# Kernel optimization log

Measured on AMD Instinct MI355X. Metric: run time of the kernel, lower is better.

## Reference

```python
import jax, jax.numpy as jnp
import numpy as np

EMB = 1024
HID = 1536
NE = 8


def setup_inputs() -> dict:
    key = jax.random.key(0)
    ks = jax.random.split(key, 8)
    B, N, E, H, ne = 4, 2048, EMB, HID, NE
    s = 1.0 / np.sqrt(E)
    sh = 1.0 / np.sqrt(H)
    return {
        "x": jax.random.normal(ks[0], (B, N, E), dtype=jnp.float32),
        "Wr": jax.random.uniform(ks[1], (E, ne), minval=-s, maxval=s, dtype=jnp.float32),
        "br": jax.random.uniform(ks[2], (ne,), minval=-s, maxval=s, dtype=jnp.float32),
        "W1": jax.random.uniform(ks[3], (ne, E, H), minval=-s, maxval=s, dtype=jnp.float32),
        "b1": jax.random.uniform(ks[4], (ne, H), minval=-s, maxval=s, dtype=jnp.float32),
        "W2": jax.random.uniform(ks[5], (ne, H, E), minval=-sh, maxval=sh, dtype=jnp.float32),
        "b2": jax.random.uniform(ks[6], (ne, E), minval=-sh, maxval=sh, dtype=jnp.float32),
        "k": 2,
    }


def reference(x, Wr, br, W1, b1, W2, b2, k):
    B, N, E = x.shape
    T = B * N
    ne = Wr.shape[1]
    flat = x.reshape(T, E)
    logits = flat @ Wr + br                      # [T, ne]
    _, topk_idx = jax.lax.top_k(logits, k)       # [T, k]
    # counts[t, e] = number of top-k slots of token t assigned to expert e
    counts = jax.nn.one_hot(topk_idx, ne, dtype=flat.dtype).sum(axis=1)  # [T, ne]
    out = jnp.zeros_like(flat)
    for e in range(ne):  # small fixed loop over experts (structurally distinct weights)
        h = jax.nn.gelu(flat @ W1[e] + b1[e], approximate=False)  # torch nn.GELU = exact erf
        y = h @ W2[e] + b2[e]
        out = out + counts[:, e:e + 1] * y
    out = out / k
    return out.reshape(B, N, E)
```

## Files before the change

### kernel.cpp

```cpp
#include <hip/hip_runtime.h>
#include <hip/hip_bf16.h>
#include <math.h>

#define T_TOK 8192
#define EMB   1024
#define HID   1536
#define NE    8
#define NBINB 64
#define BINTOK (T_TOK / NBINB)

typedef float  floatx4 __attribute__((ext_vector_type(4)));
typedef __bf16 bf16x8  __attribute__((ext_vector_type(8)));

#define WS_COUNTS   0
#define WS_OFFSETS  1024
#define WS_FLAGS    2048
#define WS_BHIST    4096
#define WS_TOKMAP   8192
#define WS_TOKLIST  270336
#define WS_YBUF     532480
#define WS_W1T      34086912
#define WS_W2T      59252736
#define WS_H        84418560
#define WS_NEEDED   135143424

__device__ __forceinline__ float eload(const void* p, size_t idx, bool f32) {
  return f32 ? ((const float*)p)[idx] : (float)(((const __bf16*)p)[idx]);
}

__device__ __forceinline__ void glds16(const void* g, void* l) {
  __builtin_amdgcn_global_load_lds(
      (const __attribute__((address_space(1))) unsigned int*)g,
      (__attribute__((address_space(3))) unsigned int*)l, 16, 0, 0);
}

__global__ __launch_bounds__(256)
void sniff_kernel(const void* p0, const void* p1, const void* p2, const void* p3,
                  const void* p4, const void* p5, const void* p6, int* flags) {
  const void* ps[7] = {p0, p1, p2, p3, p4, p5, p6};
  const int nelem[7] = {T_TOK * EMB, EMB * NE, NE, NE * EMB * HID, NE * HID, NE * HID * EMB, NE * EMB};
  int t = blockIdx.x;
  const unsigned* w = (const unsigned*)ps[t];
  int nw = nelem[t] / 2;
  if (nw > 2048) nw = 2048;
  __shared__ int s_pl, s_nz;
  if (threadIdx.x == 0) { s_pl = 0; s_nz = 0; }
  __syncthreads();
  int pl = 0, nz = 0;
  for (int i = threadIdx.x; i < nw; i += 256) {
    unsigned v = w[i];
    if (v == 0) continue;
    nz++;
    unsigned e = (v >> 23) & 0xFF;
    if (e >= 100 && e <= 150) pl++;
  }
  atomicAdd(&s_pl, pl);
  atomicAdd(&s_nz, nz);
  __syncthreads();
  if (threadIdx.x == 0) flags[t] = (2 * s_pl > s_nz) ? 1 : 0;
}

__global__ __launch_bounds__(256)
void logits_kernel(const void* __restrict__ x, const void* __restrict__ Wr,
                   const void* __restrict__ br, const int* __restrict__ kptr,
                   const int* __restrict__ flags, int* __restrict__ topk,
                   __bf16* __restrict__ xbf) {
  const bool xf32  = flags[0] != 0;
  const bool wrf32 = flags[1] != 0;
  const bool brf32 = flags[2] != 0;
  const int wave = threadIdx.x >> 6;
  const int lane = threadIdx.x & 63;
  const int t = blockIdx.x * 4 + wave;

  float xv[16];
  {
    size_t base = (size_t)t * EMB + lane * 16;
    if (xf32) {
      const float* g = (const float*)x + base;
#pragma unroll
      for (int j = 0; j < 16; ++j) xv[j] = g[j];
    } else {
      bf16x8 u = *(const bf16x8*)((const __bf16*)x + base);
      bf16x8 v = *(const bf16x8*)((const __bf16*)x + base + 8);
#pragma unroll
      for (int j = 0; j < 8; ++j) { xv[j] = (float)u[j]; xv[8 + j] = (float)v[j]; }
    }
  }
  {
    bf16x8 o0, o1;
#pragma unroll
    for (int j = 0; j < 8; ++j) { o0[j] = (__bf16)xv[j]; o1[j] = (__bf16)xv[8 + j]; }
    __bf16* xo = xbf + (size_t)t * EMB + lane * 16;
    *(bf16x8*)xo = o0;
    *(bf16x8*)(xo + 8) = o1;
  }
  float acc[NE];
#pragma unroll
  for (int e = 0; e < NE; ++e) acc[e] = 0.f;
  if (wrf32) {
#pragma unroll
    for (int j = 0; j < 16; ++j) {
      const float* wr = (const float*)Wr + (size_t)(lane * 16 + j) * NE;
#pragma unroll
      for (int e = 0; e < NE; ++e) acc[e] += xv[j] * wr[e];
    }
  } else {
#pragma unroll
    for (int j = 0; j < 16; ++j) {
      bf16x8 wr = *(const bf16x8*)((const __bf16*)Wr + (size_t)(lane * 16 + j) * NE);
#pragma unroll
      for (int e = 0; e < NE; ++e) acc[e] += xv[j] * (float)wr[e];
    }
  }
#pragma unroll
  for (int e = 0; e < NE; ++e) {
#pragma unroll
    for (int off = 32; off > 0; off >>= 1)
      acc[e] += __shfl_xor(acc[e], off, 64);
  }
  if (lane == 0) {
    int k = kptr[0];
    if (k < 1) k = 1; if (k > NE) k = NE;
    float lg[NE];
#pragma unroll
    for (int e = 0; e < NE; ++e) lg[e] = acc[e] + eload(br, e, brf32);
    for (int s = 0; s < k; ++s) {
      int bi = 0; float bv = lg[0];
#pragma unroll
      for (int e = 1; e < NE; ++e) { if (lg[e] > bv) { bv = lg[e]; bi = e; } }
      lg[bi] = -3.0e38f;
      topk[t * 8 + s] = bi;
    }
  }
}

__global__ __launch_bounds__(128)
void bin1_kernel(const int* __restrict__ topk, const int* __restrict__ kptr,
                 int* __restrict__ bhist) {
  __shared__ int lhist[NE];
  if (threadIdx.x < NE) lhist[threadIdx.x] = 0;
  __syncthreads();
  int k = kptr[0];
  if (k < 1) k = 1; if (k > NE) k = NE;
  const int t = blockIdx.x * BINTOK + threadIdx.x;
  for (int s = 0; s < k; ++s) atomicAdd(&lhist[topk[t * 8 + s] & 7], 1);
  __syncthreads();
  if (threadIdx.x < NE) bhist[blockIdx.x * NE + threadIdx.x] = lhist[threadIdx.x];
}

__global__ __launch_bounds__(256)
void scan_kernel(int* __restrict__ bhist, int* __restrict__ counts, int* __restrict__ offsets) {
  __shared__ int sh[NBINB * NE];
  __shared__ int scnt[NE];
  __shared__ int soff[NE + 1];
  const int tid = threadIdx.x;
  for (int i = tid; i < NBINB * NE; i += 256) sh[i] = bhist[i];
  __syncthreads();
  if (tid < NE) {
    int s = 0;
    for (int b = 0; b < NBINB; ++b) s += sh[b * NE + tid];
    scnt[tid] = s;
  }
  __syncthreads();
  if (tid == 0) {
    int s = 0;
    for (int e = 0; e < NE; ++e) { soff[e] = s; s += scnt[e]; }
    soff[NE] = s;
  }
  __syncthreads();
  if (tid < NE) {
    int run = soff[tid];
    for (int b = 0; b < NBINB; ++b) {
      int v = sh[b * NE + tid];
      sh[b * NE + tid] = run;
      run += v;
    }
  }
  __syncthreads();
  for (int i = tid; i < NBINB * NE; i += 256) bhist[i] = sh[i];
  if (tid < NE) counts[tid] = scnt[tid];
  if (tid < NE + 1) offsets[tid] = soff[tid];
}

__global__ __launch_bounds__(128)
void bin2_kernel(const int* __restrict__ bhist, const int* __restrict__ offsets,
                 const int* __restrict__ kptr,
                 int* __restrict__ tok_list, int* __restrict__ tokmap) {
  __shared__ int lbase[NE];
  __shared__ int lcnt[NE];
  if (threadIdx.x < NE) {
    lbase[threadIdx.x] = bhist[blockIdx.x * NE + threadIdx.x];
    lcnt[threadIdx.x] = 0;
  }
  __syncthreads();
  int k = kptr[0];
  if (k < 1) k = 1; if (k > NE) k = NE;
  const int t = blockIdx.x * BINTOK + threadIdx.x;
  for (int s = 0; s < k; ++s) {
    int e = tokmap[t * 8 + s] & 7;
    int pos = atomicAdd(&lcnt[e], 1);
    int grow = lbase[e] + pos;
    tok_list[e * T_TOK + (grow - offsets[e])] = t;
    tokmap[t * 8 + s] = (e << 16) | grow;
  }
}

__global__ __launch_bounds__(256)
void transpose2_kernel(const void* __restrict__ W1, const void* __restrict__ W2,
                       __bf16* __restrict__ w1t, __bf16* __restrict__ w2t,
                       const int* __restrict__ flags) {
  const int z = blockIdx.z;
  const void* in; __bf16* out; int K, N; bool f32;
  if (z < 8) { in = W1; out = w1t; K = EMB; N = HID; f32 = flags[3] != 0; }
  else       { in = W2; out = w2t; K = HID; N = EMB; f32 = flags[5] != 0; }
  if ((int)blockIdx.x * 64 >= N || (int)blockIdx.y * 64 >= K) return;
  __shared__ __bf16 tile[64][65];
  size_t eoff = (size_t)(z & 7) * (size_t)K * (size_t)N;
  int n0 = blockIdx.x * 64;
  int k0 = blockIdx.y * 64;
  int tx = threadIdx.x & 63;
  int ty = threadIdx.x >> 6;
#pragma unroll
  for (int i = 0; i < 16; ++i) {
    int r = i * 4 + ty;
    tile[r][tx] = (__bf16)eload(in, eoff + (size_t)(k0 + r) * N + (n0 + tx), f32);
  }
  __syncthreads();
#pragma unroll
  for (int i = 0; i < 16; ++i) {
    int r = i * 4 + ty;
    out[eoff + (size_t)(n0 + r) * K + (k0 + tx)] = tile[tx][r];
  }
}


__global__ __launch_bounds__(256, 4)
void gemm1_kernel(const __bf16* __restrict__ xbf, const __bf16* __restrict__ w1t,
                  const void* __restrict__ b1, const int* __restrict__ counts,
                  const int* __restrict__ offsets, const int* __restrict__ tok_list,
                  const int* __restrict__ flags, __bf16* __restrict__ hbuf) {
  const int flat = blockIdx.x;
  const int e   = flat & 7;
  const int idx = flat >> 3;
  const int g   = idx / 12;
  const int nT  = idx % 12;
  const int cnt = counts[e];
  const bool b1f32 = flags[4] != 0;

  __shared__ __align__(16) __bf16 As[128 * 32];
  __shared__ __align__(16) __bf16 Bs[128 * 32];

  const int wave = threadIdx.x >> 6;
  const int lane = threadIdx.x & 63;
  const int sr = lane >> 2;
  const int r0 = wave * 16 + sr;
  const int r1 = 64 + wave * 16 + sr;
  const int cg = (lane & 3) ^ ((r0 >> 1) & 3);

  const __bf16* pB0base = w1t + ((size_t)e * HID + nT * 128 + r0) * EMB + cg * 8;
  const __bf16* pB1base = w1t + ((size_t)e * HID + nT * 128 + r1) * EMB + cg * 8;

  __bf16* dA0 = As + wave * 512;
  __bf16* dA1 = As + 2048 + wave * 512;
  __bf16* dB0 = Bs + wave * 512;
  __bf16* dB1 = Bs + 2048 + wave * 512;

  const int wm = (wave & 1) * 64;
  const int wn = (wave >> 1) * 64;
  const int fr = lane & 15;
  const int fc = lane >> 4;
  int aOff[4], bOff[4];
#pragma unroll
  for (int i = 0; i < 4; ++i) { int R = wm + i * 16 + fr; aOff[i] = R * 64 + ((fc ^ ((R >> 1) & 3)) << 4); }
#pragma unroll
  for (int j = 0; j < 4; ++j) { int R = wn + j * 16 + fr; bOff[j] = R * 64 + ((fc ^ ((R >> 1) & 3)) << 4); }

  const int colBase = nT * 128 + wn + fr;
  float bv[4];
#pragma unroll
  for (int j = 0; j < 4; ++j) bv[j] = eload(b1, (size_t)e * HID + colBase + j * 16, b1f32);

  for (int mT = g; mT * 128 < cnt; mT += 16) {
    const int tokA0 = tok_list[e * T_TOK + mT * 128 + r0];
    const int tokA1 = tok_list[e * T_TOK + mT * 128 + r1];
    const __bf16* pA0 = xbf + (size_t)tokA0 * EMB + cg * 8;
    const __bf16* pA1 = xbf + (size_t)tokA1 * EMB + cg * 8;
    const __bf16* pB0 = pB0base;
    const __bf16* pB1 = pB1base;

    floatx4 acc[4][4];
#pragma unroll
    for (int i = 0; i < 4; ++i)
#pragma unroll
      for (int j = 0; j < 4; ++j) acc[i][j] = (floatx4){0.f, 0.f, 0.f, 0.f};

    for (int kb = 0; kb < EMB / 32; ++kb) {
      __syncthreads();
      glds16(pA0, dA0); glds16(pA1, dA1);
      glds16(pB0, dB0); glds16(pB1, dB1);
      pA0 += 32; pA1 += 32; pB0 += 32; pB1 += 32;
      __syncthreads();
      bf16x8 af[4], bfr[4];
#pragma unroll
      for (int i = 0; i < 4; ++i) af[i]  = *(const bf16x8*)((const char*)As + aOff[i]);
#pragma unroll
      for (int j = 0; j < 4; ++j) bfr[j] = *(const bf16x8*)((const char*)Bs + bOff[j]);
#pragma unroll
      for (int i = 0; i < 4; ++i)
#pragma unroll
        for (int j = 0; j < 4; ++j)
          acc[i][j] = __builtin_amdgcn_mfma_f32_16x16x32_bf16(af[i], bfr[j], acc[i][j], 0, 0, 0);
    }

    const int hBase = offsets[e] + mT * 128;
#pragma unroll
    for (int i = 0; i < 4; ++i) {
      const int rowLoc = wm + i * 16 + fc * 4;
#pragma unroll
      for (int r = 0; r < 4; ++r) {
        const int row = rowLoc + r;
        if (mT * 128 + row < cnt) {
          __bf16* hp = hbuf + (size_t)(hBase + row) * HID + colBase;
#pragma unroll
          for (int j = 0; j < 4; ++j) {
            float v = acc[i][j][r] + bv[j];
            float gl = 0.5f * v * (1.0f + erff(v * 0.70710678118654752f));
            hp[j * 16] = (__bf16)gl;
          }
        }
      }
    }
  }
}

__global__ __launch_bounds__(256, 4)
void gemm2_kernel(const __bf16* __restrict__ hbuf, const __bf16* __restrict__ w2t,
                  const void* __restrict__ b2, const int* __restrict__ counts,
                  const int* __restrict__ offsets, const int* __restrict__ flags,
                  __bf16* __restrict__ ybuf) {
  const int flat = blockIdx.x;
  const int e   = flat & 7;
  const int idx = flat >> 3;
  const int g   = idx >> 3;
  const int nT  = idx & 7;
  const int cnt = counts[e];
  const bool b2f32 = flags[6] != 0;

  __shared__ __align__(16) __bf16 As[128 * 32];
  __shared__ __align__(16) __bf16 Bs[128 * 32];

  const int wave = threadIdx.x >> 6;
  const int lane = threadIdx.x & 63;
  const int sr = lane >> 2;
  const int r0 = wave * 16 + sr;
  const int r1 = 64 + wave * 16 + sr;
  const int cg = (lane & 3) ^ ((r0 >> 1) & 3);

  const __bf16* pB0base = w2t + ((size_t)e * EMB + nT * 128 + r0) * HID + cg * 8;
  const __bf16* pB1base = w2t + ((size_t)e * EMB + nT * 128 + r1) * HID + cg * 8;

  __bf16* dA0 = As + wave * 512;
  __bf16* dA1 = As + 2048 + wave * 512;
  __bf16* dB0 = Bs + wave * 512;
  __bf16* dB1 = Bs + 2048 + wave * 512;

  const int wm = (wave & 1) * 64;
  const int wn = (wave >> 1) * 64;
  const int fr = lane & 15;
  const int fc = lane >> 4;
  int aOff[4], bOff[4];
#pragma unroll
  for (int i = 0; i < 4; ++i) { int R = wm + i * 16 + fr; aOff[i] = R * 64 + ((fc ^ ((R >> 1) & 3)) << 4); }
#pragma unroll
  for (int j = 0; j < 4; ++j) { int R = wn + j * 16 + fr; bOff[j] = R * 64 + ((fc ^ ((R >> 1) & 3)) << 4); }

  const int colBase = nT * 128 + wn + fr;
  float bv[4];
#pragma unroll
  for (int j = 0; j < 4; ++j) bv[j] = eload(b2, (size_t)e * EMB + colBase + j * 16, b2f32);

  for (int mT = g; mT * 128 < cnt; mT += 16) {
    const int rowBase = offsets[e] + mT * 128;
    const __bf16* pA0 = hbuf + (size_t)(rowBase + r0) * HID + cg * 8;
    const __bf16* pA1 = hbuf + (size_t)(rowBase + r1) * HID + cg * 8;
    const __bf16* pB0 = pB0base;
    const __bf16* pB1 = pB1base;

    floatx4 acc[4][4];
#pragma unroll
    for (int i = 0; i < 4; ++i)
#pragma unroll
      for (int j = 0; j < 4; ++j) acc[i][j] = (floatx4){0.f, 0.f, 0.f, 0.f};

    for (int kb = 0; kb < HID / 32; ++kb) {
      __syncthreads();
      glds16(pA0, dA0); glds16(pA1, dA1);
      glds16(pB0, dB0); glds16(pB1, dB1);
      pA0 += 32; pA1 += 32; pB0 += 32; pB1 += 32;
      __syncthreads();
      bf16x8 af[4], bfr[4];
#pragma unroll
      for (int i = 0; i < 4; ++i) af[i]  = *(const bf16x8*)((const char*)As + aOff[i]);
#pragma unroll
      for (int j = 0; j < 4; ++j) bfr[j] = *(const bf16x8*)((const char*)Bs + bOff[j]);
#pragma unroll
      for (int i = 0; i < 4; ++i)
#pragma unroll
        for (int j = 0; j < 4; ++j)
          acc[i][j] = __builtin_amdgcn_mfma_f32_16x16x32_bf16(af[i], bfr[j], acc[i][j], 0, 0, 0);
    }

#pragma unroll
    for (int i = 0; i < 4; ++i) {
      const int rowLoc = wm + i * 16 + fc * 4;
#pragma unroll
      for (int r = 0; r < 4; ++r) {
        const int row = rowLoc + r;
        if (mT * 128 + row < cnt) {
          __bf16* yp = ybuf + (size_t)(rowBase + row) * EMB + colBase;
#pragma unroll
          for (int j = 0; j < 4; ++j)
            yp[j * 16] = (__bf16)(acc[i][j][r] + bv[j]);
        }
      }
    }
  }
}

__global__ __launch_bounds__(256)
void combine_kernel(const __bf16* __restrict__ ybuf, const int* __restrict__ tokmap,
                    const int* __restrict__ kptr, const int* __restrict__ flags,
                    void* __restrict__ out) {
  const bool f32 = flags[0] != 0;
  const int wave = threadIdx.x >> 6;
  const int lane = threadIdx.x & 63;
  const int t = blockIdx.x * 4 + wave;
  int k = kptr[0];
  if (k < 1) k = 1; if (k > NE) k = NE;
  const float invk = 1.0f / (float)k;
  int rows[NE];
  for (int s = 0; s < k; ++s) rows[s] = tokmap[t * 8 + s] & 0xFFFF;
#pragma unroll
  for (int c = 0; c < 2; ++c) {
    const int i = c * 512 + lane * 8;
    float a[8];
#pragma unroll
    for (int j = 0; j < 8; ++j) a[j] = 0.f;
    for (int s = 0; s < k; ++s) {
      bf16x8 y = *(const bf16x8*)(ybuf + (size_t)rows[s] * EMB + i);
#pragma unroll
      for (int j = 0; j < 8; ++j) a[j] += (float)y[j];
    }
    if (f32) {
      float* op = (float*)out + (size_t)t * EMB + i;
      float4 u = {a[0] * invk, a[1] * invk, a[2] * invk, a[3] * invk};
      float4 v = {a[4] * invk, a[5] * invk, a[6] * invk, a[7] * invk};
      *(float4*)op = u;
      *(float4*)(op + 4) = v;
    } else {
      bf16x8 o;
#pragma unroll
      for (int j = 0; j < 8; ++j) o[j] = (__bf16)(a[j] * invk);
      *(bf16x8*)((__bf16*)out + (size_t)t * EMB + i) = o;
    }
  }
}

extern "C" void kernel_launch(void* const* d_in, const int* in_sizes, int n_in,
                              void* d_out, int out_size, void* d_ws, size_t ws_size,
                              hipStream_t stream) {
  (void)in_sizes; (void)n_in; (void)out_size;
  if (ws_size < (size_t)WS_NEEDED) return;

  const void* x  = d_in[0];
  const void* Wr = d_in[1];
  const void* br = d_in[2];
  const void* W1 = d_in[3];
  const void* b1 = d_in[4];
  const void* W2 = d_in[5];
  const void* b2 = d_in[6];
  const int* kptr = (const int*)d_in[7];

  char* ws = (char*)d_ws;
  int*    counts   = (int*)(ws + WS_COUNTS);
  int*    offsets  = (int*)(ws + WS_OFFSETS);
  int*    flags    = (int*)(ws + WS_FLAGS);
  int*    bhist    = (int*)(ws + WS_BHIST);
  int*    tokmap   = (int*)(ws + WS_TOKMAP);
  int*    tok_list = (int*)(ws + WS_TOKLIST);
  __bf16* ybuf     = (__bf16*)(ws + WS_YBUF);
  __bf16* xbf      = (__bf16*)(ws + WS_YBUF);
  __bf16* w1t      = (__bf16*)(ws + WS_W1T);
  __bf16* w2t      = (__bf16*)(ws + WS_W2T);
  __bf16* hbuf     = (__bf16*)(ws + WS_H);

  hipMemsetAsync(ws + WS_TOKLIST, 0, NE * T_TOK * 4, stream);

  sniff_kernel<<<dim3(7), 256, 0, stream>>>(x, Wr, br, W1, b1, W2, b2, flags);

  transpose2_kernel<<<dim3(HID / 64, HID / 64, 16), 256, 0, stream>>>(W1, W2, w1t, w2t, flags);

  logits_kernel<<<dim3(T_TOK / 4), 256, 0, stream>>>(x, Wr, br, kptr, flags, tokmap, xbf);
  bin1_kernel<<<dim3(NBINB), 128, 0, stream>>>(tokmap, kptr, bhist);
  scan_kernel<<<dim3(1), 256, 0, stream>>>(bhist, counts, offsets);
  bin2_kernel<<<dim3(NBINB), 128, 0, stream>>>(bhist, offsets, kptr, tok_list, tokmap);

  gemm1_kernel<<<dim3(8 * 16 * 12), 256, 0, stream>>>(
      xbf, w1t, b1, counts, offsets, tok_list, flags, hbuf);
  gemm2_kernel<<<dim3(8 * 16 * 8), 256, 0, stream>>>(
      hbuf, w2t, b2, counts, offsets, flags, ybuf);

  combine_kernel<<<dim3(T_TOK / 4), 256, 0, stream>>>(ybuf, tokmap, kptr, flags, d_out);
}
```

Baseline: 401.1 us.

## Double GEMM K-tile to 64 with XOR swizzle and vectorize weight transpose

```diff
diff --git a/kernel.cpp b/kernel.cpp
--- a/kernel.cpp
+++ b/kernel.cpp
@@ -214,22 +214,43 @@
   if (z < 8) { in = W1; out = w1t; K = EMB; N = HID; f32 = flags[3] != 0; }
   else       { in = W2; out = w2t; K = HID; N = EMB; f32 = flags[5] != 0; }
   if ((int)blockIdx.x * 64 >= N || (int)blockIdx.y * 64 >= K) return;
-  __shared__ __bf16 tile[64][65];
+  __shared__ __bf16 tile[64][66];
   size_t eoff = (size_t)(z & 7) * (size_t)K * (size_t)N;
-  int n0 = blockIdx.x * 64;
-  int k0 = blockIdx.y * 64;
-  int tx = threadIdx.x & 63;
-  int ty = threadIdx.x >> 6;
-#pragma unroll
-  for (int i = 0; i < 16; ++i) {
-    int r = i * 4 + ty;
-    tile[r][tx] = (__bf16)eload(in, eoff + (size_t)(k0 + r) * N + (n0 + tx), f32);
-  }
-  __syncthreads();
-#pragma unroll
-  for (int i = 0; i < 16; ++i) {
-    int r = i * 4 + ty;
-    out[eoff + (size_t)(n0 + r) * K + (k0 + tx)] = tile[tx][r];
+  const int n0 = blockIdx.x * 64;
+  const int k0 = blockIdx.y * 64;
+  const int tid = threadIdx.x;
+
+  if (f32) {
+    const int nn = (tid & 15) * 4;
+    const int kr = tid >> 4;
+#pragma unroll
+    for (int p = 0; p < 4; ++p) {
+      const int k = kr + p * 16;
+      float4 v = *(const float4*)((const float*)in + eoff + (size_t)(k0 + k) * N + n0 + nn);
+      tile[k][nn + 0] = (__bf16)v.x; tile[k][nn + 1] = (__bf16)v.y;
+      tile[k][nn + 2] = (__bf16)v.z; tile[k][nn + 3] = (__bf16)v.w;
+    }
+  } else {
+    const int nn = (tid & 7) * 8;
+    const int kr = tid >> 3;
+#pragma unroll
+    for (int p = 0; p < 2; ++p) {
+      const int k = kr + p * 32;
+      bf16x8 v = *(const bf16x8*)((const __bf16*)in + eoff + (size_t)(k0 + k) * N + n0 + nn);
+#pragma unroll
+      for (int j = 0; j < 8; ++j) tile[k][nn + j] = v[j];
+    }
+  }
+  __syncthreads();
+  const int kk = (tid & 7) * 8;
+  const int nr = tid >> 3;
+#pragma unroll
+  for (int p = 0; p < 2; ++p) {
+    const int n = nr + p * 32;
+    bf16x8 o;
+#pragma unroll
+    for (int j = 0; j < 8; ++j) o[j] = tile[kk + j][n];
+    *(bf16x8*)(out + eoff + (size_t)(n0 + n) * K + k0 + kk) = o;
   }
 }
 
@@ -247,33 +268,40 @@
   const int cnt = counts[e];
   const bool b1f32 = flags[4] != 0;
 
-  __shared__ __align__(16) __bf16 As[128 * 32];
-  __shared__ __align__(16) __bf16 Bs[128 * 32];
+  __shared__ __align__(16) __bf16 As[128 * 64];
+  __shared__ __align__(16) __bf16 Bs[128 * 64];
 
   const int wave = threadIdx.x >> 6;
   const int lane = threadIdx.x & 63;
-  const int sr = lane >> 2;
-  const int r0 = wave * 16 + sr;
-  const int r1 = 64 + wave * 16 + sr;
-  const int cg = (lane & 3) ^ ((r0 >> 1) & 3);
-
-  const __bf16* pB0base = w1t + ((size_t)e * HID + nT * 128 + r0) * EMB + cg * 8;
-  const __bf16* pB1base = w1t + ((size_t)e * HID + nT * 128 + r1) * EMB + cg * 8;
-
-  __bf16* dA0 = As + wave * 512;
-  __bf16* dA1 = As + 2048 + wave * 512;
-  __bf16* dB0 = Bs + wave * 512;
-  __bf16* dB1 = Bs + 2048 + wave * 512;
+  const int lrow = lane >> 3;
+  const int cgs  = (lane & 7) ^ lrow;
+
+  int Rst[4];
+#pragma unroll
+  for (int q = 0; q < 4; ++q) Rst[q] = (q * 4 + wave) * 8 + lrow;
+
+  const __bf16* pB[4];
+#pragma unroll
+  for (int q = 0; q < 4; ++q)
+    pB[q] = w1t + ((size_t)e * HID + nT * 128 + Rst[q]) * EMB + cgs * 8;
 
   const int wm = (wave & 1) * 64;
   const int wn = (wave >> 1) * 64;
   const int fr = lane & 15;
   const int fc = lane >> 4;
-  int aOff[4], bOff[4];
-#pragma unroll
-  for (int i = 0; i < 4; ++i) { int R = wm + i * 16 + fr; aOff[i] = R * 64 + ((fc ^ ((R >> 1) & 3)) << 4); }
-#pragma unroll
-  for (int j = 0; j < 4; ++j) { int R = wn + j * 16 + fr; bOff[j] = R * 64 + ((fc ^ ((R >> 1) & 3)) << 4); }
+  int aOff0[4], aOff1[4], bOff0[4], bOff1[4];
+#pragma unroll
+  for (int i = 0; i < 4; ++i) {
+    int R = wm + i * 16 + fr;
+    aOff0[i] = R * 128 + (((fc)     ^ (R & 7)) << 4);
+    aOff1[i] = R * 128 + (((fc + 4) ^ (R & 7)) << 4);
+  }
+#pragma unroll
+  for (int j = 0; j < 4; ++j) {
+    int R = wn + j * 16 + fr;
+    bOff0[j] = R * 128 + (((fc)     ^ (R & 7)) << 4);
+    bOff1[j] = R * 128 + (((fc + 4) ^ (R & 7)) << 4);
+  }
 
   const int colBase = nT * 128 + wn + fr;
   float bv[4];
@@ -281,12 +309,12 @@
   for (int j = 0; j < 4; ++j) bv[j] = eload(b1, (size_t)e * HID + colBase + j * 16, b1f32);
 
   for (int mT = g; mT * 128 < cnt; mT += 16) {
-    const int tokA0 = tok_list[e * T_TOK + mT * 128 + r0];
-    const int tokA1 = tok_list[e * T_TOK + mT * 128 + r1];
-    const __bf16* pA0 = xbf + (size_t)tokA0 * EMB + cg * 8;
-    const __bf16* pA1 = xbf + (size_t)tokA1 * EMB + cg * 8;
-    const __bf16* pB0 = pB0base;
-    const __bf16* pB1 = pB1base;
+    const __bf16* pA[4];
+#pragma unroll
+    for (int q = 0; q < 4; ++q) {
+      const int tok = tok_list[e * T_TOK + mT * 128 + Rst[q]];
+      pA[q] = xbf + (size_t)tok * EMB + cgs * 8;
+    }
 
     floatx4 acc[4][4];
 #pragma unroll
@@ -294,17 +322,27 @@
 #pragma unroll
       for (int j = 0; j < 4; ++j) acc[i][j] = (floatx4){0.f, 0.f, 0.f, 0.f};
 
-    for (int kb = 0; kb < EMB / 32; ++kb) {
+    for (int kb = 0; kb < EMB / 64; ++kb) {
       __syncthreads();
-      glds16(pA0, dA0); glds16(pA1, dA1);
-      glds16(pB0, dB0); glds16(pB1, dB1);
-      pA0 += 32; pA1 += 32; pB0 += 32; pB1 += 32;
+#pragma unroll
+      for (int q = 0; q < 4; ++q) glds16(pA[q] + (size_t)kb * 64, As + (q * 4 + wave) * 512);
+#pragma unroll
+      for (int q = 0; q < 4; ++q) glds16(pB[q] + (size_t)kb * 64, Bs + (q * 4 + wave) * 512);
       __syncthreads();
       bf16x8 af[4], bfr[4];
 #pragma unroll
-      for (int i = 0; i < 4; ++i) af[i]  = *(const bf16x8*)((const char*)As + aOff[i]);
-#pragma unroll
-      for (int j = 0; j < 4; ++j) bfr[j] = *(const bf16x8*)((const char*)Bs + bOff[j]);
+      for (int i = 0; i < 4; ++i) af[i]  = *(const bf16x8*)((const char*)As + aOff0[i]);
+#pragma unroll
+      for (int j = 0; j < 4; ++j) bfr[j] = *(const bf16x8*)((const char*)Bs + bOff0[j]);
+#pragma unroll
+      for (int i = 0; i < 4; ++i)
+#pragma unroll
+        for (int j = 0; j < 4; ++j)
+          acc[i][j] = __builtin_amdgcn_mfma_f32_16x16x32_bf16(af[i], bfr[j], acc[i][j], 0, 0, 0);
+#pragma unroll
+      for (int i = 0; i < 4; ++i) af[i]  = *(const bf16x8*)((const char*)As + aOff1[i]);
+#pragma unroll
+      for (int j = 0; j < 4; ++j) bfr[j] = *(const bf16x8*)((const char*)Bs + bOff1[j]);
 #pragma unroll
       for (int i = 0; i < 4; ++i)
 #pragma unroll
@@ -346,33 +384,40 @@
   const int cnt = counts[e];
   const bool b2f32 = flags[6] != 0;
 
-  __shared__ __align__(16) __bf16 As[128 * 32];
-  __shared__ __align__(16) __bf16 Bs[128 * 32];
+  __shared__ __align__(16) __bf16 As[128 * 64];
+  __shared__ __align__(16) __bf16 Bs[128 * 64];
 
   const int wave = threadIdx.x >> 6;
   const int lane = threadIdx.x & 63;
-  const int sr = lane >> 2;
-  const int r0 = wave * 16 + sr;
-  const int r1 = 64 + wave * 16 + sr;
-  const int cg = (lane & 3) ^ ((r0 >> 1) & 3);
-
-  const __bf16* pB0base = w2t + ((size_t)e * EMB + nT * 128 + r0) * HID + cg * 8;
-  const __bf16* pB1base = w2t + ((size_t)e * EMB + nT * 128 + r1) * HID + cg * 8;
-
-  __bf16* dA0 = As + wave * 512;
-  __bf16* dA1 = As + 2048 + wave * 512;
-  __bf16* dB0 = Bs + wave * 512;
-  __bf16* dB1 = Bs + 2048 + wave * 512;
+  const int lrow = lane >> 3;
+  const int cgs  = (lane & 7) ^ lrow;
+
+  int Rst[4];
+#pragma unroll
+  for (int q = 0; q < 4; ++q) Rst[q] = (q * 4 + wave) * 8 + lrow;
+
+  const __bf16* pB[4];
+#pragma unroll
+  for (int q = 0; q < 4; ++q)
+    pB[q] = w2t + ((size_t)e * EMB + nT * 128 + Rst[q]) * HID + cgs * 8;
 
   const int wm = (wave & 1) * 64;
   const int wn = (wave >> 1) * 64;
   const int fr = lane & 15;
   const int fc = lane >> 4;
-  int aOff[4], bOff[4];
-#pragma unroll
-  for (int i = 0; i < 4; ++i) { int R = wm + i * 16 + fr; aOff[i] = R * 64 + ((fc ^ ((R >> 1) & 3)) << 4); }
-#pragma unroll
-  for (int j = 0; j < 4; ++j) { int R = wn + j * 16 + fr; bOff[j] = R * 64 + ((fc ^ ((R >> 1) & 3)) << 4); }
+  int aOff0[4], aOff1[4], bOff0[4], bOff1[4];
+#pragma unroll
+  for (int i = 0; i < 4; ++i) {
+    int R = wm + i * 16 + fr;
+    aOff0[i] = R * 128 + (((fc)     ^ (R & 7)) << 4);
+    aOff1[i] = R * 128 + (((fc + 4) ^ (R & 7)) << 4);
+  }
+#pragma unroll
+  for (int j = 0; j < 4; ++j) {
+    int R = wn + j * 16 + fr;
+    bOff0[j] = R * 128 + (((fc)     ^ (R & 7)) << 4);
+    bOff1[j] = R * 128 + (((fc + 4) ^ (R & 7)) << 4);
+  }
 
   const int colBase = nT * 128 + wn + fr;
   float bv[4];
@@ -381,10 +426,10 @@
 
   for (int mT = g; mT * 128 < cnt; mT += 16) {
     const int rowBase = offsets[e] + mT * 128;
-    const __bf16* pA0 = hbuf + (size_t)(rowBase + r0) * HID + cg * 8;
-    const __bf16* pA1 = hbuf + (size_t)(rowBase + r1) * HID + cg * 8;
-    const __bf16* pB0 = pB0base;
-    const __bf16* pB1 = pB1base;
+    const __bf16* pA[4];
+#pragma unroll
+    for (int q = 0; q < 4; ++q)
+      pA[q] = hbuf + (size_t)(rowBase + Rst[q]) * HID + cgs * 8;
 
     floatx4 acc[4][4];
 #pragma unroll
@@ -392,17 +437,27 @@
 #pragma unroll
       for (int j = 0; j < 4; ++j) acc[i][j] = (floatx4){0.f, 0.f, 0.f, 0.f};
 
-    for (int kb = 0; kb < HID / 32; ++kb) {
+    for (int kb = 0; kb < HID / 64; ++kb) {
       __syncthreads();
-      glds16(pA0, dA0); glds16(pA1, dA1);
-      glds16(pB0, dB0); glds16(pB1, dB1);
-      pA0 += 32; pA1 += 32; pB0 += 32; pB1 += 32;
+#pragma unroll
+      for (int q = 0; q < 4; ++q) glds16(pA[q] + (size_t)kb * 64, As + (q * 4 + wave) * 512);
+#pragma unroll
+      for (int q = 0; q < 4; ++q) glds16(pB[q] + (size_t)kb * 64, Bs + (q * 4 + wave) * 512);
       __syncthreads();
       bf16x8 af[4], bfr[4];
 #pragma unroll
-      for (int i = 0; i < 4; ++i) af[i]  = *(const bf16x8*)((const char*)As + aOff[i]);
-#pragma unroll
-      for (int j = 0; j < 4; ++j) bfr[j] = *(const bf16x8*)((const char*)Bs + bOff[j]);
+      for (int i = 0; i < 4; ++i) af[i]  = *(const bf16x8*)((const char*)As + aOff0[i]);
+#pragma unroll
+      for (int j = 0; j < 4; ++j) bfr[j] = *(const bf16x8*)((const char*)Bs + bOff0[j]);
+#pragma unroll
+      for (int i = 0; i < 4; ++i)
+#pragma unroll
+        for (int j = 0; j < 4; ++j)
+          acc[i][j] = __builtin_amdgcn_mfma_f32_16x16x32_bf16(af[i], bfr[j], acc[i][j], 0, 0, 0);
+#pragma unroll
+      for (int i = 0; i < 4; ++i) af[i]  = *(const bf16x8*)((const char*)As + aOff1[i]);
+#pragma unroll
+      for (int j = 0; j < 4; ++j) bfr[j] = *(const bf16x8*)((const char*)Bs + bOff1[j]);
 #pragma unroll
       for (int i = 0; i < 4; ++i)
 #pragma unroll
```

Result: faster. 368.5 us (-8.1%).
